# Optimization experiments

Hardware: AMD Instinct MI355X
Metric: run time of the kernel (lower is better)

## Reference

```python
import jax, jax.numpy as jnp
import numpy as np

B, Q, K, DIM, H = 16, 256, 4096, 1024, 16
HD = DIM // H          # head_dim = 64
SCALE = float(np.sqrt(HD))
MAX_QUERIES = 64       # keep_first=True -> kept Q' = MAX_QUERIES + 1


def setup_inputs() -> dict:
    key = jax.random.key(0)
    ks = jax.random.split(key, 8)
    s = 1.0 / np.sqrt(DIM)
    return {
        "q": jax.random.normal(ks[0], (B, Q, DIM), jnp.float32),
        "k": jax.random.normal(ks[1], (B, K, DIM), jnp.float32),
        "v": jax.random.normal(ks[2], (B, K, DIM), jnp.float32),
        "Wq": jax.random.normal(ks[3], (DIM, DIM), jnp.float32) * s,
        "Wk": jax.random.normal(ks[4], (DIM, DIM), jnp.float32) * s,
        "Wv": jax.random.normal(ks[5], (DIM, DIM), jnp.float32) * s,
        "Wo": jax.random.normal(ks[6], (DIM, DIM), jnp.float32) * s,
        "bo": jnp.zeros((DIM,), jnp.float32),
    }


def _split_heads(x):  # [B, L, DIM] -> [B, L, H, HD]
    return x.reshape(x.shape[0], x.shape[1], H, HD)


def reference(q, k, v, Wq, Wk, Wv, Wo, bo):
    # QKV projections (no bias, matching qkv_bias=False; torch Linear is x @ W.T)
    qh = _split_heads(q @ Wq.T)   # [B,Q,H,HD]
    kh = _split_heads(k @ Wk.T)   # [B,K,H,HD]
    vh = _split_heads(v @ Wv.T)   # [B,K,H,HD]

    dots = jnp.einsum("bqhc,bkhc->bhqk", qh / SCALE, kh)  # [B,H,Q,K]

    # select_queries with keep_first=True: stats on detached dots over queries 1:
    sg = jax.lax.stop_gradient(dots)[:, :, 1:, :]          # [B,H,Q-1,K]
    stats = jax.nn.softmax(sg, axis=-2)                    # softmax over query axis
    score = stats.max(axis=(1, 3))                         # amax over (H, K) -> [B, Q-1]
    _, idx = jax.lax.top_k(score, MAX_QUERIES)             # [B, MAX_QUERIES]
    keep = jnp.concatenate(
        [jnp.zeros((dots.shape[0], 1), idx.dtype), idx + 1], axis=-1
    )                                                      # [B, Q'] with Q' = MAX_QUERIES+1

    dots_sel = jnp.take_along_axis(dots, keep[:, None, :, None], axis=2)  # [B,H,Q',K]

    # Competitive softmax: normalize over the (kept) query axis
    attn = jax.nn.softmax(dots_sel, axis=2)                # [B,H,Q',K]

    out = jnp.einsum("bhqk,bkhc->bqhc", attn, vh)          # [B,Q',H,HD]
    out = out.reshape(out.shape[0], out.shape[1], DIM)     # [B,Q',DIM]
    out = out @ Wo.T + bo
    return out, keep
```

## Files before the change

kernel.cpp:

```cpp
#include <hip/hip_runtime.h>
#include <hip/hip_bf16.h>
#include <math.h>

#define B_ 16
#define Q_ 256
#define K_ 4096
#define DIM_ 1024
#define H_ 16
#define HD_ 64
#define MQ_ 64
#define QP_ 65
#define SCALE_INV 0.125f

typedef unsigned short u16;
typedef __attribute__((ext_vector_type(8))) short bf16x8;
typedef __attribute__((ext_vector_type(8))) _Float16 f16x8;
typedef __attribute__((ext_vector_type(8))) short s16x8;
typedef __attribute__((ext_vector_type(4))) float f32x4;

__device__ __forceinline__ u16 f2bf_rne(float f) {
  unsigned u = __float_as_uint(f);
  u += 0x7fffu + ((u >> 16) & 1u);
  return (u16)(u >> 16);
}
__device__ __forceinline__ float bf2f(u16 h) {
  return __uint_as_float(((unsigned)h) << 16);
}
__device__ __forceinline__ u16 f2h_bits(float f) {
  _Float16 h = (_Float16)f;
  return *(u16*)&h;
}
__device__ __forceinline__ f16x8 as_f16x8(s16x8 v) {
  return __builtin_bit_cast(f16x8, v);
}
__device__ __forceinline__ void gload16(const void* g, void* l) {
  __builtin_amdgcn_global_load_lds(
      (const __attribute__((address_space(1))) unsigned int*)g,
      (__attribute__((address_space(3))) unsigned int*)l, 16, 0, 0);
}

__global__ __launch_bounds__(256) void split_bf16(
    const float* __restrict__ x, u16* __restrict__ hi, u16* __restrict__ lo,
    long n8, int wlo) {
  long i = (long)blockIdx.x * 256 + threadIdx.x;
  const long stride = (long)gridDim.x * 256;
  for (; i < n8; i += stride) {
    const float4 a = ((const float4*)x)[2 * i];
    const float4 b = ((const float4*)x)[2 * i + 1];
    const float xs[8] = {a.x, a.y, a.z, a.w, b.x, b.y, b.z, b.w};
    u16 h[8], l[8];
#pragma unroll
    for (int j = 0; j < 8; ++j) {
      h[j] = f2bf_rne(xs[j]);
      l[j] = f2bf_rne(xs[j] - bf2f(h[j]));
    }
    uint4 hv;
    hv.x = h[0] | ((unsigned)h[1] << 16);
    hv.y = h[2] | ((unsigned)h[3] << 16);
    hv.z = h[4] | ((unsigned)h[5] << 16);
    hv.w = h[6] | ((unsigned)h[7] << 16);
    ((uint4*)hi)[i] = hv;
    if (wlo) {
      uint4 lv;
      lv.x = l[0] | ((unsigned)l[1] << 16);
      lv.y = l[2] | ((unsigned)l[3] << 16);
      lv.z = l[4] | ((unsigned)l[5] << 16);
      lv.w = l[6] | ((unsigned)l[7] << 16);
      ((uint4*)lo)[i] = lv;
    }
  }
}

template <int NPROD, int OUTM>
__global__ __launch_bounds__(256) void mfma_gemm_f32a(
    const float* __restrict__ Af,
    const u16* __restrict__ Bhp, const u16* __restrict__ Blp,
    float* __restrict__ C, u16* __restrict__ ChH, u16* __restrict__ ChL) {
  __shared__ u16 Ah_s[128 * 32];
  __shared__ u16 Bh_s[128 * 32];
  __shared__ u16 Al_s[NPROD >= 3 ? 128 * 32 : 16];
  __shared__ u16 Bl_s[NPROD >= 3 ? 128 * 32 : 16];
  const int t = threadIdx.x;
  const int wave = t >> 6;
  const int lane = t & 63;
  const int wr = wave >> 1;
  const int wc = wave & 1;

  int bx = blockIdx.x, by = blockIdx.y;
  if (gridDim.x == 8 && (gridDim.y & 7) == 0) {
    const int flat = by * 8 + bx;
    const int c = flat & 7;
    const int j = flat >> 3;
    by = (j >> 3) * 8 + c;
    bx = j & 7;
  }
  const int n0 = bx * 128;
  const int m0 = by * 128;

  const int sr0 = wave * 32 + (lane >> 2);
  const int sr1 = sr0 + 16;
  const int sw0 = ((sr0 ^ (sr0 >> 2)) & 3) ^ (lane & 3);
  const int sw1 = ((sr1 ^ (sr1 >> 2)) & 3) ^ (lane & 3);
  const size_t gB0 = (size_t)(n0 + sr0) * DIM_ + sw0 * 8;
  const size_t gB1 = (size_t)(n0 + sr1) * DIM_ + sw1 * 8;
  u16* const lB0 = &Bh_s[(wave * 32) * 32];
  u16* const lB1 = &Bh_s[(wave * 32 + 16) * 32];
  u16* const lBl0 = &Bl_s[(wave * 32) * 32];
  u16* const lBl1 = &Bl_s[(wave * 32 + 16) * 32];

  const int ar = t >> 1;
  const int ac0 = (t & 1) * 2;
  const int swzr = (ar ^ (ar >> 2)) & 3;
  const int sl0 = (ac0 ^ swzr) * 8;
  const int sl1 = ((ac0 + 1) ^ swzr) * 8;
  const size_t gA = (size_t)(m0 + ar) * DIM_ + ac0 * 8;

  int aoff[4], boff[4];
#pragma unroll
  for (int m = 0; m < 4; ++m) {
    const int r = wr * 64 + m * 16 + (lane & 15);
    const int p = ((r ^ (r >> 2)) & 3) ^ (lane >> 4);
    aoff[m] = r * 32 + p * 8;
  }
#pragma unroll
  for (int n = 0; n < 4; ++n) {
    const int r = wc * 64 + n * 16 + (lane & 15);
    const int p = ((r ^ (r >> 2)) & 3) ^ (lane >> 4);
    boff[n] = r * 32 + p * 8;
  }

  f32x4 acc[4][4];
#pragma unroll
  for (int m = 0; m < 4; ++m)
#pragma unroll
    for (int n = 0; n < 4; ++n) acc[m][n] = (f32x4)(0.f);

  for (int k0 = 0; k0 < DIM_; k0 += 32) {
    gload16(Bhp + gB0 + k0, lB0);
    gload16(Bhp + gB1 + k0, lB1);
    if (NPROD >= 3) {
      gload16(Blp + gB0 + k0, lBl0);
      gload16(Blp + gB1 + k0, lBl1);
    }
    {
      const float4 a0 = *(const float4*)&Af[gA + k0];
      const float4 a1 = *(const float4*)&Af[gA + k0 + 4];
      const float4 a2 = *(const float4*)&Af[gA + k0 + 8];
      const float4 a3 = *(const float4*)&Af[gA + k0 + 12];
      const float xs[16] = {a0.x, a0.y, a0.z, a0.w, a1.x, a1.y, a1.z, a1.w,
                            a2.x, a2.y, a2.z, a2.w, a3.x, a3.y, a3.z, a3.w};
      u16 h[16], l[16];
#pragma unroll
      for (int j = 0; j < 16; ++j) {
        h[j] = f2bf_rne(xs[j]);
        if (NPROD >= 3) l[j] = f2bf_rne(xs[j] - bf2f(h[j]));
      }
      uint4 hv0, hv1;
      hv0.x = h[0] | ((unsigned)h[1] << 16);  hv0.y = h[2] | ((unsigned)h[3] << 16);
      hv0.z = h[4] | ((unsigned)h[5] << 16);  hv0.w = h[6] | ((unsigned)h[7] << 16);
      hv1.x = h[8] | ((unsigned)h[9] << 16);  hv1.y = h[10] | ((unsigned)h[11] << 16);
      hv1.z = h[12] | ((unsigned)h[13] << 16); hv1.w = h[14] | ((unsigned)h[15] << 16);
      *(uint4*)&Ah_s[ar * 32 + sl0] = hv0;
      *(uint4*)&Ah_s[ar * 32 + sl1] = hv1;
      if (NPROD >= 3) {
        uint4 lv0, lv1;
        lv0.x = l[0] | ((unsigned)l[1] << 16);  lv0.y = l[2] | ((unsigned)l[3] << 16);
        lv0.z = l[4] | ((unsigned)l[5] << 16);  lv0.w = l[6] | ((unsigned)l[7] << 16);
        lv1.x = l[8] | ((unsigned)l[9] << 16);  lv1.y = l[10] | ((unsigned)l[11] << 16);
        lv1.z = l[12] | ((unsigned)l[13] << 16); lv1.w = l[14] | ((unsigned)l[15] << 16);
        *(uint4*)&Al_s[ar * 32 + sl0] = lv0;
        *(uint4*)&Al_s[ar * 32 + sl1] = lv1;
      }
    }
    __syncthreads();
    {
      bf16x8 af[4], bfr[4];
#pragma unroll
      for (int m = 0; m < 4; ++m) af[m] = *(const bf16x8*)&Ah_s[aoff[m]];
#pragma unroll
      for (int n = 0; n < 4; ++n) bfr[n] = *(const bf16x8*)&Bh_s[boff[n]];
#pragma unroll
      for (int m = 0; m < 4; ++m)
#pragma unroll
        for (int n = 0; n < 4; ++n)
          acc[m][n] = __builtin_amdgcn_mfma_f32_16x16x32_bf16(
              af[m], bfr[n], acc[m][n], 0, 0, 0);
      if (NPROD >= 3) {
#pragma unroll
        for (int n = 0; n < 4; ++n) bfr[n] = *(const bf16x8*)&Bl_s[boff[n]];
#pragma unroll
        for (int m = 0; m < 4; ++m)
#pragma unroll
          for (int n = 0; n < 4; ++n)
            acc[m][n] = __builtin_amdgcn_mfma_f32_16x16x32_bf16(
                af[m], bfr[n], acc[m][n], 0, 0, 0);
#pragma unroll
        for (int m = 0; m < 4; ++m) af[m] = *(const bf16x8*)&Al_s[aoff[m]];
#pragma unroll
        for (int n = 0; n < 4; ++n) bfr[n] = *(const bf16x8*)&Bh_s[boff[n]];
#pragma unroll
        for (int m = 0; m < 4; ++m)
#pragma unroll
          for (int n = 0; n < 4; ++n)
            acc[m][n] = __builtin_amdgcn_mfma_f32_16x16x32_bf16(
                af[m], bfr[n], acc[m][n], 0, 0, 0);
      }
    }
    __syncthreads();
  }
#pragma unroll
  for (int m = 0; m < 4; ++m) {
    const int row = m0 + wr * 64 + m * 16 + (lane >> 4) * 4;
#pragma unroll
    for (int n = 0; n < 4; ++n) {
      const int col = n0 + wc * 64 + n * 16 + (lane & 15);
#pragma unroll
      for (int j = 0; j < 4; ++j) {
        const size_t idx = (size_t)(row + j) * DIM_ + col;
        const float a = acc[m][n][j];
        if (OUTM & 1) C[idx] = a;
        if (OUTM & 4) {
          _Float16 hi = (_Float16)a;
          ChH[idx] = *(u16*)&hi;
          if (OUTM & 8) {
            _Float16 lo = (_Float16)(a - (float)hi);
            ChL[idx] = *(u16*)&lo;
          }
        }
      }
    }
  }
}

#define GM 128
#define GN 128
#define GK 16

__global__ __launch_bounds__(256) void gemm_nt(
    const float* __restrict__ A, const float* __restrict__ W,
    float* __restrict__ C, int M, const float* __restrict__ bias,
    u16* __restrict__ hiOut, u16* __restrict__ loOut) {
  __shared__ float As[GK][GM + 4];
  __shared__ float Ws[GK][GN + 4];
  const int t = threadIdx.x;
  const int m0 = blockIdx.x * GM;
  const int n0 = blockIdx.y * GN;
  const int lrow = t >> 2;
  const int lq = (t & 3) * 4;
  const int tm = (t >> 4) * 8;
  const int tn = (t & 15) * 8;
  float acc[8][8];
#pragma unroll
  for (int i = 0; i < 8; ++i)
#pragma unroll
    for (int j = 0; j < 8; ++j) acc[i][j] = 0.f;

  for (int k0 = 0; k0 < DIM_; k0 += GK) {
#pragma unroll
    for (int half = 0; half < 2; ++half) {
      const int row = lrow + half * 64;
      const int gm = m0 + row;
      float4 av = make_float4(0.f, 0.f, 0.f, 0.f);
      if (gm < M) av = *(const float4*)&A[(size_t)gm * DIM_ + k0 + lq];
      As[lq + 0][row] = av.x; As[lq + 1][row] = av.y;
      As[lq + 2][row] = av.z; As[lq + 3][row] = av.w;
      const int gn = n0 + row;
      const float4 wv = *(const float4*)&W[(size_t)gn * DIM_ + k0 + lq];
      Ws[lq + 0][row] = wv.x; Ws[lq + 1][row] = wv.y;
      Ws[lq + 2][row] = wv.z; Ws[lq + 3][row] = wv.w;
    }
    __syncthreads();
#pragma unroll
    for (int kk = 0; kk < GK; ++kk) {
      float a[8], bb[8];
      *(float4*)&a[0] = *(const float4*)&As[kk][tm];
      *(float4*)&a[4] = *(const float4*)&As[kk][tm + 4];
      *(float4*)&bb[0] = *(const float4*)&Ws[kk][tn];
      *(float4*)&bb[4] = *(const float4*)&Ws[kk][tn + 4];
#pragma unroll
      for (int i = 0; i < 8; ++i)
#pragma unroll
        for (int j = 0; j < 8; ++j)
          acc[i][j] = fmaf(a[i], bb[j], acc[i][j]);
    }
    __syncthreads();
  }
#pragma unroll
  for (int i = 0; i < 8; ++i) {
    const int gm = m0 + tm + i;
    if (gm < M) {
      float vals[8];
#pragma unroll
      for (int j = 0; j < 8; ++j) {
        vals[j] = acc[i][j];
        if (bias) vals[j] += bias[n0 + tn + j];
      }
#pragma unroll
      for (int j = 0; j < 8; j += 4) {
        float4 ov;
        ov.x = vals[j + 0]; ov.y = vals[j + 1];
        ov.z = vals[j + 2]; ov.w = vals[j + 3];
        *(float4*)&C[(size_t)gm * DIM_ + n0 + tn + j] = ov;
      }
      if (hiOut) {
        u16 h[8], l[8];
#pragma unroll
        for (int j = 0; j < 8; ++j) {
          _Float16 hh = (_Float16)vals[j];
          _Float16 ll = (_Float16)(vals[j] - (float)hh);
          h[j] = *(u16*)&hh;
          l[j] = *(u16*)&ll;
        }
        uint4 hv, lv;
        hv.x = h[0] | ((unsigned)h[1] << 16); hv.y = h[2] | ((unsigned)h[3] << 16);
        hv.z = h[4] | ((unsigned)h[5] << 16); hv.w = h[6] | ((unsigned)h[7] << 16);
        lv.x = l[0] | ((unsigned)l[1] << 16); lv.y = l[2] | ((unsigned)l[3] << 16);
        lv.z = l[4] | ((unsigned)l[5] << 16); lv.w = l[6] | ((unsigned)l[7] << 16);
        *(uint4*)&hiOut[(size_t)gm * DIM_ + n0 + tn] = hv;
        *(uint4*)&loOut[(size_t)gm * DIM_ + n0 + tn] = lv;
      }
    }
  }
}

__device__ __forceinline__ unsigned fflip(float x) {
  const unsigned u = __float_as_uint(x);
  return (u & 0x80000000u) ? ~u : (u | 0x80000000u);
}

#define AKT 64

__global__ __launch_bounds__(256) void pass_a_mfma(
    const u16* __restrict__ qhH, const u16* __restrict__ qhL,
    const u16* __restrict__ khH, const u16* __restrict__ khL,
    unsigned* __restrict__ sbuf) {
  __shared__ u16 KsH[AKT * 72];
  __shared__ u16 KsL[AKT * 72];
  __shared__ float red[4][2 * AKT];
  const int bx = blockIdx.x;
  const int b = bx >> 7;
  const int h = (bx >> 3) & 15;
  const int ks0 = (bx & 7) * (K_ / 8);
  const int t = threadIdx.x;
  const int w = t >> 6;
  const int l = t & 63;
  const int g = l >> 4;
  const int a15 = l & 15;

  f16x8 qA[2][4][2];
#pragma unroll
  for (int mt = 0; mt < 4; ++mt) {
    const int qrow = w * 64 + mt * 16 + a15;
    const size_t base = ((size_t)(b * Q_ + qrow)) * DIM_ + h * HD_;
#pragma unroll
    for (int ks = 0; ks < 2; ++ks) {
      qA[0][mt][ks] = *(const f16x8*)&qhH[base + ks * 32 + g * 8];
      qA[1][mt][ks] = *(const f16x8*)&qhL[base + ks * 32 + g * 8];
    }
  }
  float rmax[4][4];
#pragma unroll
  for (int mt = 0; mt < 4; ++mt)
#pragma unroll
    for (int j = 0; j < 4; ++j) rmax[mt][j] = -3.4e38f;

  for (int k0 = ks0; k0 < ks0 + K_ / 8; k0 += AKT) {
    uint4 sH[2], sL[2];
    int sr[2], sc[2];
#pragma unroll
    for (int s = 0; s < 2; ++s) {
      const int c = t + 256 * s;
      sr[s] = c >> 3;
      sc[s] = c & 7;
      const size_t gidx =
          ((size_t)(b * K_ + k0 + sr[s])) * DIM_ + h * HD_ + sc[s] * 8;
      sH[s] = *(const uint4*)&khH[gidx];
      sL[s] = *(const uint4*)&khL[gidx];
    }
    __syncthreads();
#pragma unroll
    for (int s = 0; s < 2; ++s) {
      *(uint4*)&KsH[sr[s] * 72 + sc[s] * 8] = sH[s];
      *(uint4*)&KsL[sr[s] * 72 + sc[s] * 8] = sL[s];
    }
    __syncthreads();

    f32x4 acc[4][4];
#pragma unroll
    for (int mt = 0; mt < 4; ++mt)
#pragma unroll
      for (int kt = 0; kt < 4; ++kt) acc[mt][kt] = (f32x4)(0.f);
#pragma unroll
    for (int ks = 0; ks < 2; ++ks) {
#pragma unroll
      for (int kt = 0; kt < 4; ++kt) {
        const f16x8 bH =
            *(const f16x8*)&KsH[(kt * 16 + a15) * 72 + ks * 32 + g * 8];
        const f16x8 bL =
            *(const f16x8*)&KsL[(kt * 16 + a15) * 72 + ks * 32 + g * 8];
#pragma unroll
        for (int mt = 0; mt < 4; ++mt) {
          acc[mt][kt] = __builtin_amdgcn_mfma_f32_16x16x32_f16(
              qA[0][mt][ks], bH, acc[mt][kt], 0, 0, 0);
          acc[mt][kt] = __builtin_amdgcn_mfma_f32_16x16x32_f16(
              qA[0][mt][ks], bL, acc[mt][kt], 0, 0, 0);
          acc[mt][kt] = __builtin_amdgcn_mfma_f32_16x16x32_f16(
              qA[1][mt][ks], bH, acc[mt][kt], 0, 0, 0);
        }
      }
    }
#pragma unroll
    for (int mt = 0; mt < 4; ++mt)
#pragma unroll
      for (int kt = 0; kt < 4; ++kt) acc[mt][kt] = acc[mt][kt] * 0.125f;

    float cmax[4];
#pragma unroll
    for (int kt = 0; kt < 4; ++kt) {
      float m = -3.4e38f;
#pragma unroll
      for (int mt = 0; mt < 4; ++mt)
#pragma unroll
        for (int j = 0; j < 4; ++j) {
          const bool ex = (w == 0) & (mt == 0) & (g == 0) & (j == 0);
          if (!ex) m = fmaxf(m, acc[mt][kt][j]);
        }
      m = fmaxf(m, __shfl_xor(m, 16, 64));
      m = fmaxf(m, __shfl_xor(m, 32, 64));
      cmax[kt] = m;
    }
    if (l < 16) {
#pragma unroll
      for (int kt = 0; kt < 4; ++kt) red[w][kt * 16 + l] = cmax[kt];
    }
    __syncthreads();
#pragma unroll
    for (int kt = 0; kt < 4; ++kt)
      cmax[kt] = fmaxf(fmaxf(red[0][kt * 16 + a15], red[1][kt * 16 + a15]),
                       fmaxf(red[2][kt * 16 + a15], red[3][kt * 16 + a15]));
    float csum[4];
#pragma unroll
    for (int kt = 0; kt < 4; ++kt) {
      float s = 0.f;
#pragma unroll
      for (int mt = 0; mt < 4; ++mt)
#pragma unroll
        for (int j = 0; j < 4; ++j) {
          const bool ex = (w == 0) & (mt == 0) & (g == 0) & (j == 0);
          if (!ex) s += __expf(acc[mt][kt][j] - cmax[kt]);
        }
      s += __shfl_xor(s, 16, 64);
      s += __shfl_xor(s, 32, 64);
      csum[kt] = s;
    }
    if (l < 16) {
#pragma unroll
      for (int kt = 0; kt < 4; ++kt) red[w][AKT + kt * 16 + l] = csum[kt];
    }
    __syncthreads();
    float lse[4];
#pragma unroll
    for (int kt = 0; kt < 4; ++kt) {
      const float s = red[0][AKT + kt * 16 + a15] + red[1][AKT + kt * 16 + a15] +
                      red[2][AKT + kt * 16 + a15] + red[3][AKT + kt * 16 + a15];
      lse[kt] = cmax[kt] + logf(s);
    }
#pragma unroll
    for (int mt = 0; mt < 4; ++mt)
#pragma unroll
      for (int j = 0; j < 4; ++j) {
        float v = -3.4e38f;
#pragma unroll
        for (int kt = 0; kt < 4; ++kt)
          v = fmaxf(v, acc[mt][kt][j] - lse[kt]);
        v = fmaxf(v, __shfl_xor(v, 1, 64));
        v = fmaxf(v, __shfl_xor(v, 2, 64));
        v = fmaxf(v, __shfl_xor(v, 4, 64));
        v = fmaxf(v, __shfl_xor(v, 8, 64));
        rmax[mt][j] = fmaxf(rmax[mt][j], v);
      }
  }
  if (a15 == 0) {
#pragma unroll
    for (int mt = 0; mt < 4; ++mt)
#pragma unroll
      for (int j = 0; j < 4; ++j) {
        const int qi = w * 64 + mt * 16 + g * 4 + j;
        if (qi > 0) atomicMax(&sbuf[b * Q_ + qi], fflip(rmax[mt][j]));
      }
  }
}

#define KT 64
#define DC 32
#define KSPLIT 8

__global__ __launch_bounds__(256) void pass_a(
    const float* __restrict__ qh, const float* __restrict__ kh,
    unsigned* __restrict__ sbuf) {
  __shared__ float qs[DC][Q_ + 4];
  __shared__ float ksm[DC][KT + 4];
  __shared__ float red[32][KT + 1];
  __shared__ float cmax[KT];
  __shared__ float clse[KT];
  const int blk = blockIdx.x;
  const int b = blk >> 7;
  const int h = (blk >> 3) & 15;
  const int ks0 = (blk & 7) * (K_ / KSPLIT);
  const int t = threadIdx.x;
  const int tq = t >> 3;
  const int tk = t & 7;
  float rmax[8];
#pragma unroll
  for (int i = 0; i < 8; ++i) rmax[i] = -3.4e38f;

  for (int k0 = ks0; k0 < ks0 + K_ / KSPLIT; k0 += KT) {
    float acc[8][8];
#pragma unroll
    for (int i = 0; i < 8; ++i)
#pragma unroll
      for (int j = 0; j < 8; ++j) acc[i][j] = 0.f;

    for (int dc = 0; dc < HD_; dc += DC) {
      {
        const float* src = &qh[((size_t)(b * Q_ + t)) * DIM_ + h * HD_ + dc];
#pragma unroll
        for (int u = 0; u < DC / 4; ++u) {
          const float4 vv = *(const float4*)&src[u * 4];
          qs[u * 4 + 0][t] = vv.x * SCALE_INV;
          qs[u * 4 + 1][t] = vv.y * SCALE_INV;
          qs[u * 4 + 2][t] = vv.z * SCALE_INV;
          qs[u * 4 + 3][t] = vv.w * SCALE_INV;
        }
      }
      {
        const int r = t >> 2;
        const int qd = (t & 3) * 8;
        const float* src =
            &kh[((size_t)(b * K_ + k0 + r)) * DIM_ + h * HD_ + dc + qd];
#pragma unroll
        for (int u = 0; u < 2; ++u) {
          const float4 vv = *(const float4*)&src[u * 4];
          ksm[qd + u * 4 + 0][r] = vv.x; ksm[qd + u * 4 + 1][r] = vv.y;
          ksm[qd + u * 4 + 2][r] = vv.z; ksm[qd + u * 4 + 3][r] = vv.w;
        }
      }
      __syncthreads();
#pragma unroll
      for (int d = 0; d < DC; ++d) {
        float a[8], bb[8];
        *(float4*)&a[0] = *(const float4*)&qs[d][tq * 8];
        *(float4*)&a[4] = *(const float4*)&qs[d][tq * 8 + 4];
        *(float4*)&bb[0] = *(const float4*)&ksm[d][tk * 8];
        *(float4*)&bb[4] = *(const float4*)&ksm[d][tk * 8 + 4];
#pragma unroll
        for (int i = 0; i < 8; ++i)
#pragma unroll
          for (int j = 0; j < 8; ++j)
            acc[i][j] = fmaf(a[i], bb[j], acc[i][j]);
      }
      __syncthreads();
    }
#pragma unroll
    for (int j = 0; j < 8; ++j) {
      float m = -3.4e38f;
#pragma unroll
      for (int i = 0; i < 8; ++i) {
        if (tq == 0 && i == 0) continue;
        m = fmaxf(m, acc[i][j]);
      }
      red[tq][tk * 8 + j] = m;
    }
    __syncthreads();
    if (t < KT) {
      float m = -3.4e38f;
      for (int g = 0; g < 32; ++g) m = fmaxf(m, red[g][t]);
      cmax[t] = m;
    }
    __syncthreads();
#pragma unroll
    for (int j = 0; j < 8; ++j) {
      const float m = cmax[tk * 8 + j];
      float s = 0.f;
#pragma unroll
      for (int i = 0; i < 8; ++i) {
        if (tq == 0 && i == 0) continue;
        s += __expf(acc[i][j] - m);
      }
      red[tq][tk * 8 + j] = s;
    }
    __syncthreads();
    if (t < KT) {
      float s = 0.f;
      for (int g = 0; g < 32; ++g) s += red[g][t];
      clse[t] = cmax[t] + logf(s);
    }
    __syncthreads();
#pragma unroll
    for (int i = 0; i < 8; ++i) {
      float v = -3.4e38f;
#pragma unroll
      for (int j = 0; j < 8; ++j) v = fmaxf(v, acc[i][j] - clse[tk * 8 + j]);
      v = fmaxf(v, __shfl_xor(v, 1, 64));
      v = fmaxf(v, __shfl_xor(v, 2, 64));
      v = fmaxf(v, __shfl_xor(v, 4, 64));
      rmax[i] = fmaxf(rmax[i], v);
    }
    __syncthreads();
  }
  if (tk == 0) {
#pragma unroll
    for (int i = 0; i < 8; ++i) {
      const int qi = tq * 8 + i;
      if (qi > 0) atomicMax(&sbuf[b * Q_ + qi], fflip(rmax[i]));
    }
  }
}

__global__ void topk_kernel(const unsigned* __restrict__ sbuf,
                            int* __restrict__ keep, float* __restrict__ keepf) {
  const int b = blockIdx.x;
  const int lane = threadIdx.x;
  unsigned long long pk[4];
#pragma unroll
  for (int j = 0; j < 4; ++j) {
    const int q = 1 + lane + 64 * j;
    if (q <= 255) {
      const unsigned s = sbuf[b * Q_ + q];
      pk[j] = (((unsigned long long)s) << 32) | (unsigned)(256 - q);
    } else {
      pk[j] = 0ull;
    }
  }
  if (lane == 0) { keep[b * QP_] = 0; keepf[b * QP_] = 0.f; }
  for (int it = 0; it < MQ_; ++it) {
    unsigned long long best = pk[0];
#pragma unroll
    for (int j = 1; j < 4; ++j) best = (pk[j] > best) ? pk[j] : best;
    for (int m = 1; m < 64; m <<= 1) {
      const unsigned long long o = __shfl_xor(best, m, 64);
      best = (o > best) ? o : best;
    }
    const int q = 256 - (int)(best & 0xffffffffu);
#pragma unroll
    for (int j = 0; j < 4; ++j)
      if (pk[j] == best) pk[j] = 0ull;
    if (lane == 0) {
      keep[b * QP_ + 1 + it] = q;
      keepf[b * QP_ + 1 + it] = (float)q;
    }
  }
}

#define PSPL 4

__global__ __launch_bounds__(256) void pass_b_mfma(
    const float* __restrict__ qh, const u16* __restrict__ khb,
    const u16* __restrict__ vhb, const int* __restrict__ keep,
    float* __restrict__ part) {
  __shared__ __align__(16) char SH[72960];
  u16* const Qs = (u16*)SH;
  u16* const Ks = (u16*)(SH + 11520);
  u16* const Vs = (u16*)(SH + 29952);
  u16* const Ps = (u16*)(SH + 47360);
  float* const osum = (float*)(SH + 11520);

  const int bx = blockIdx.x;
  const int b = bx >> 6;
  const int h = (bx >> 2) & 15;
  const int sp = bx & 3;
  const int t = threadIdx.x;
  const int w = t >> 6;
  const int l = t & 63;
  const int g = l >> 4;
  const int a15 = l & 15;

  for (int idx = t; idx < 80 * 8; idx += 256) {
    const int row = idx >> 3, ch = idx & 7;
    uint4 pk;
    if (row < QP_) {
      const int kq = keep[b * QP_ + row];
      const float* src = &qh[((size_t)(b * Q_ + kq)) * DIM_ + h * HD_ + ch * 8];
      const float4 x0 = *(const float4*)&src[0];
      const float4 x1 = *(const float4*)&src[4];
      pk.x = f2h_bits(x0.x * SCALE_INV) | ((unsigned)f2h_bits(x0.y * SCALE_INV) << 16);
      pk.y = f2h_bits(x0.z * SCALE_INV) | ((unsigned)f2h_bits(x0.w * SCALE_INV) << 16);
      pk.z = f2h_bits(x1.x * SCALE_INV) | ((unsigned)f2h_bits(x1.y * SCALE_INV) << 16);
      pk.w = f2h_bits(x1.z * SCALE_INV) | ((unsigned)f2h_bits(x1.w * SCALE_INV) << 16);
    } else {
      pk = make_uint4(0, 0, 0, 0);
    }
    *(uint4*)&Qs[row * 72 + ch * 8] = pk;
  }
  __syncthreads();

  f32x4 oacc[5][4];
#pragma unroll
  for (int mt = 0; mt < 5; ++mt)
#pragma unroll
    for (int dt = 0; dt < 4; ++dt) oacc[mt][dt] = (f32x4)(0.f);

  const int kt0 = sp * (K_ / PSPL);
  for (int kt = 0; kt < K_ / PSPL; kt += 128) {
    const int k0 = kt0 + kt;
    uint4 kreg[4], vreg[4];
    int srow[4], sch[4];
#pragma unroll
    for (int s = 0; s < 4; ++s) {
      const int c = t + 256 * s;
      srow[s] = c >> 3;
      sch[s] = c & 7;
      const size_t gidx =
          ((size_t)(b * K_ + k0 + srow[s])) * DIM_ + h * HD_ + sch[s] * 8;
      kreg[s] = *(const uint4*)&khb[gidx];
      vreg[s] = *(const uint4*)&vhb[gidx];
    }
    __syncthreads();
#pragma unroll
    for (int s = 0; s < 4; ++s) {
      *(uint4*)&Ks[srow[s] * 72 + sch[s] * 8] = kreg[s];
      uint2 v0; v0.x = vreg[s].x; v0.y = vreg[s].y;
      uint2 v1; v1.x = vreg[s].z; v1.y = vreg[s].w;
      *(uint2*)&Vs[srow[s] * 68 + sch[s] * 8] = v0;
      *(uint2*)&Vs[srow[s] * 68 + sch[s] * 8 + 4] = v1;
    }
    __syncthreads();

    f32x4 S[5][2];
#pragma unroll
    for (int mt = 0; mt < 5; ++mt)
#pragma unroll
      for (int nt = 0; nt < 2; ++nt) S[mt][nt] = (f32x4)(0.f);
#pragma unroll
    for (int kk = 0; kk < 2; ++kk) {
      f16x8 aq[5];
#pragma unroll
      for (int mt = 0; mt < 5; ++mt)
        aq[mt] = *(const f16x8*)&Qs[(mt * 16 + a15) * 72 + kk * 32 + g * 8];
#pragma unroll
      for (int nt = 0; nt < 2; ++nt) {
        const f16x8 bk =
            *(const f16x8*)&Ks[(w * 32 + nt * 16 + a15) * 72 + kk * 32 + g * 8];
#pragma unroll
        for (int mt = 0; mt < 5; ++mt)
          S[mt][nt] = __builtin_amdgcn_mfma_f32_16x16x32_f16(aq[mt], bk,
                                                             S[mt][nt], 0, 0, 0);
      }
    }
#pragma unroll
    for (int nt = 0; nt < 2; ++nt) {
      float m = -3.4e38f;
#pragma unroll
      for (int mt = 0; mt < 5; ++mt)
#pragma unroll
        for (int j = 0; j < 4; ++j) {
          const bool valid = (mt < 4) | ((g == 0) & (j == 0));
          if (valid) m = fmaxf(m, S[mt][nt][j]);
        }
      m = fmaxf(m, __shfl_xor(m, 16, 64));
      m = fmaxf(m, __shfl_xor(m, 32, 64));
      float s = 0.f;
#pragma unroll
      for (int mt = 0; mt < 5; ++mt)
#pragma unroll
        for (int j = 0; j < 4; ++j) {
          const bool valid = (mt < 4) | ((g == 0) & (j == 0));
          const float p = valid ? __expf(S[mt][nt][j] - m) : 0.f;
          S[mt][nt][j] = p;
          s += p;
        }
      s += __shfl_xor(s, 16, 64);
      s += __shfl_xor(s, 32, 64);
      const float r = 1.f / s;
#pragma unroll
      for (int mt = 0; mt < 5; ++mt)
#pragma unroll
        for (int j = 0; j < 4; ++j)
          Ps[w * 3200 + (mt * 16 + g * 4 + j) * 40 + nt * 16 + a15] =
              f2h_bits(S[mt][nt][j] * r);
    }
    f16x8 ap[5];
#pragma unroll
    for (int mt = 0; mt < 5; ++mt)
      ap[mt] = *(const f16x8*)&Ps[w * 3200 + (mt * 16 + a15) * 40 + g * 8];
#pragma unroll
    for (int dt = 0; dt < 4; ++dt) {
      s16x8 bv;
#pragma unroll
      for (int e = 0; e < 8; ++e)
        bv[e] = (short)Vs[(w * 32 + g * 8 + e) * 68 + dt * 16 + a15];
#pragma unroll
      for (int mt = 0; mt < 5; ++mt)
        oacc[mt][dt] = __builtin_amdgcn_mfma_f32_16x16x32_f16(
            ap[mt], as_f16x8(bv), oacc[mt][dt], 0, 0, 0);
    }
  }

#pragma unroll
  for (int dt = 0; dt < 4; ++dt) {
    __syncthreads();
#pragma unroll
    for (int mt = 0; mt < 5; ++mt)
#pragma unroll
      for (int j = 0; j < 4; ++j)
        osum[w * 1360 + (mt * 16 + g * 4 + j) * 17 + a15] = oacc[mt][dt][j];
    __syncthreads();
    for (int idx = t; idx < QP_ * 16; idx += 256) {
      const int q = idx >> 4, c = idx & 15;
      const float sm = osum[q * 17 + c] + osum[1360 + q * 17 + c] +
                       osum[2720 + q * 17 + c] + osum[4080 + q * 17 + c];
      part[(((size_t)sp * B_ + b) * QP_ + q) * DIM_ + h * 64 + dt * 16 + c] = sm;
    }
  }
}

__global__ __launch_bounds__(256) void pass_b(
    const float* __restrict__ qh, const float* __restrict__ kh,
    const float* __restrict__ vh, const int* __restrict__ keep,
    float* __restrict__ part) {
  __shared__ float qs[QP_][HD_ + 4];
  __shared__ float kv[KT][HD_ + 4];
  __shared__ float att[QP_][KT + 4];
  __shared__ float cmax[KT];
  __shared__ float crcp[KT];
  const int bx = blockIdx.x;
  const int b = bx >> 6;
  const int h = (bx >> 2) & 15;
  const int sp = bx & 3;
  const int t = threadIdx.x;

  if (t < QP_) {
    const int kq = keep[b * QP_ + t];
    const float* src = &qh[((size_t)(b * Q_ + kq)) * DIM_ + h * HD_];
#pragma unroll
    for (int u = 0; u < HD_ / 4; ++u) {
      float4 vv = *(const float4*)&src[u * 4];
      vv.x *= SCALE_INV; vv.y *= SCALE_INV;
      vv.z *= SCALE_INV; vv.w *= SCALE_INV;
      *(float4*)&qs[t][u * 4] = vv;
    }
  }
  const int c = t & 63;
  const int jg = t >> 6;
  const int j0 = jg * 17;
  const int j1 = (jg == 3) ? QP_ : (j0 + 17);
  const int j2 = t >> 2;
  const int cg = (t & 3) * 16;
  const int r = t >> 2;
  const int qd = (t & 3) * 16;
  float oacc[16], oacc2[16];
#pragma unroll
  for (int u = 0; u < 16; ++u) { oacc[u] = 0.f; oacc2[u] = 0.f; }

  __syncthreads();

  const int kbeg = sp * (K_ / PSPL);
  const int kend = kbeg + K_ / PSPL;
  for (int k0 = kbeg; k0 < kend; k0 += KT) {
    {
      const float* src = &kh[((size_t)(b * K_ + k0 + r)) * DIM_ + h * HD_ + qd];
#pragma unroll
      for (int u = 0; u < 4; ++u)
        *(float4*)&kv[r][qd + u * 4] = *(const float4*)&src[u * 4];
    }
    __syncthreads();
    {
      float4 kr[16];
#pragma unroll
      for (int u = 0; u < 16; ++u) kr[u] = *(const float4*)&kv[c][u * 4];
      for (int j = j0; j < j1; ++j) {
        float4 s4 = make_float4(0.f, 0.f, 0.f, 0.f);
#pragma unroll
        for (int u = 0; u < 16; ++u) {
          const float4 qv = *(const float4*)&qs[j][u * 4];
          s4.x = fmaf(qv.x, kr[u].x, s4.x);
          s4.y = fmaf(qv.y, kr[u].y, s4.y);
          s4.z = fmaf(qv.z, kr[u].z, s4.z);
          s4.w = fmaf(qv.w, kr[u].w, s4.w);
        }
        att[j][c] = (s4.x + s4.y) + (s4.z + s4.w);
      }
    }
    __syncthreads();
    {
      const float* src = &vh[((size_t)(b * K_ + k0 + r)) * DIM_ + h * HD_ + qd];
#pragma unroll
      for (int u = 0; u < 4; ++u)
        *(float4*)&kv[r][qd + u * 4] = *(const float4*)&src[u * 4];
      if (t < KT) {
        float m = att[0][t];
        for (int j = 1; j < QP_; ++j) m = fmaxf(m, att[j][t]);
        float s = 0.f;
        for (int j = 0; j < QP_; ++j) s += __expf(att[j][t] - m);
        cmax[t] = m;
        crcp[t] = 1.f / s;
      }
    }
    __syncthreads();
    for (int e = t; e < QP_ * KT; e += 256) {
      const int jj = e >> 6;
      const int cc = e & 63;
      att[jj][cc] = __expf(att[jj][cc] - cmax[cc]) * crcp[cc];
    }
    __syncthreads();
    {
      for (int ck = 0; ck < KT; ++ck) {
        const float a = att[j2][ck];
#pragma unroll
        for (int u = 0; u < 4; ++u) {
          const float4 vv = *(const float4*)&kv[ck][cg + u * 4];
          oacc[u * 4 + 0] = fmaf(a, vv.x, oacc[u * 4 + 0]);
          oacc[u * 4 + 1] = fmaf(a, vv.y, oacc[u * 4 + 1]);
          oacc[u * 4 + 2] = fmaf(a, vv.z, oacc[u * 4 + 2]);
          oacc[u * 4 + 3] = fmaf(a, vv.w, oacc[u * 4 + 3]);
        }
      }
      if (t < 4) {
        const int cg2 = t * 16;
        for (int ck = 0; ck < KT; ++ck) {
          const float a = att[64][ck];
#pragma unroll
          for (int u = 0; u < 4; ++u) {
            const float4 vv = *(const float4*)&kv[ck][cg2 + u * 4];
            oacc2[u * 4 + 0] = fmaf(a, vv.x, oacc2[u * 4 + 0]);
            oacc2[u * 4 + 1] = fmaf(a, vv.y, oacc2[u * 4 + 1]);
            oacc2[u * 4 + 2] = fmaf(a, vv.z, oacc2[u * 4 + 2]);
            oacc2[u * 4 + 3] = fmaf(a, vv.w, oacc2[u * 4 + 3]);
          }
        }
      }
    }
    __syncthreads();
  }
  {
    float* dst =
        &part[(((size_t)sp * B_ + b) * QP_ + j2) * DIM_ + h * HD_ + cg];
    *(float4*)&dst[0] = make_float4(oacc[0], oacc[1], oacc[2], oacc[3]);
    *(float4*)&dst[4] = make_float4(oacc[4], oacc[5], oacc[6], oacc[7]);
    *(float4*)&dst[8] = make_float4(oacc[8], oacc[9], oacc[10], oacc[11]);
    *(float4*)&dst[12] = make_float4(oacc[12], oacc[13], oacc[14], oacc[15]);
    if (t < 4) {
      float* dst2 =
          &part[(((size_t)sp * B_ + b) * QP_ + 64) * DIM_ + h * HD_ + t * 16];
      *(float4*)&dst2[0] = make_float4(oacc2[0], oacc2[1], oacc2[2], oacc2[3]);
      *(float4*)&dst2[4] = make_float4(oacc2[4], oacc2[5], oacc2[6], oacc2[7]);
      *(float4*)&dst2[8] = make_float4(oacc2[8], oacc2[9], oacc2[10], oacc2[11]);
      *(float4*)&dst2[12] = make_float4(oacc2[12], oacc2[13], oacc2[14], oacc2[15]);
    }
  }
}

__global__ __launch_bounds__(256) void reduce_part(
    const float* __restrict__ part, float* __restrict__ opre) {
  const long n4 = (long)B_ * QP_ * DIM_ / 4;
  const long i = (long)blockIdx.x * 256 + threadIdx.x;
  if (i >= n4) return;
  float4 s = ((const float4*)part)[i];
#pragma unroll
  for (int sp = 1; sp < PSPL; ++sp) {
    const float4 p = ((const float4*)part)[(long)sp * n4 + i];
    s.x += p.x; s.y += p.y; s.z += p.z; s.w += p.w;
  }
  ((float4*)opre)[i] = s;
}

extern "C" void kernel_launch(void* const* d_in, const int* in_sizes, int n_in,
                              void* d_out, int out_size, void* d_ws, size_t ws_size,
                              hipStream_t stream) {
  const float* q  = (const float*)d_in[0];
  const float* k  = (const float*)d_in[1];
  const float* v  = (const float*)d_in[2];
  const float* Wq = (const float*)d_in[3];
  const float* Wk = (const float*)d_in[4];
  const float* Wv = (const float*)d_in[5];
  const float* Wo = (const float*)d_in[6];
  const float* bo = (const float*)d_in[7];
  float* out = (float*)d_out;

  char* base = (char*)d_ws;
  size_t off = 0;
  auto alloc = [&](size_t bytes) {
    char* p = base + off;
    off = (off + bytes + 255) & ~(size_t)255;
    return (void*)p;
  };
  float* qh   = (float*)alloc((size_t)B_ * Q_ * DIM_ * 4);
  float* opre = (float*)alloc((size_t)B_ * QP_ * DIM_ * 4);
  unsigned* sbuf = (unsigned*)alloc((size_t)B_ * Q_ * 4);
  int* keep   = (int*)alloc((size_t)B_ * QP_ * 4);
  const size_t common_off = off;
  u16* qhH = (u16*)alloc((size_t)B_ * Q_ * DIM_ * 2);
  u16* qhL = (u16*)alloc((size_t)B_ * Q_ * DIM_ * 2);
  u16* khH = (u16*)alloc((size_t)B_ * K_ * DIM_ * 2);
  u16* khL = (u16*)alloc((size_t)B_ * K_ * DIM_ * 2);
  u16* vhH = (u16*)alloc((size_t)B_ * K_ * DIM_ * 2);
  u16* wHi = (u16*)alloc((size_t)DIM_ * DIM_ * 2);
  u16* wLo = (u16*)alloc((size_t)DIM_ * DIM_ * 2);
  float* partBig = (float*)alloc((size_t)PSPL * B_ * QP_ * DIM_ * 4);
  const bool big = (off <= ws_size);
  float* keepf = out + (size_t)B_ * QP_ * DIM_;
  const dim3 blk(256);

  hipMemsetAsync(sbuf, 0, B_ * Q_ * sizeof(unsigned), stream);

  if (big) {
    const long nW8 = (long)DIM_ * DIM_ / 8;
    split_bf16<<<512, blk, 0, stream>>>(Wk, wHi, wLo, nW8, 1);
    mfma_gemm_f32a<3, 12><<<dim3(DIM_ / 128, B_ * K_ / 128), blk, 0, stream>>>(
        k, wHi, wLo, nullptr, khH, khL);
    split_bf16<<<512, blk, 0, stream>>>(Wv, wHi, nullptr, nW8, 0);
    mfma_gemm_f32a<1, 4><<<dim3(DIM_ / 128, B_ * K_ / 128), blk, 0, stream>>>(
        v, wHi, nullptr, nullptr, vhH, nullptr);
    gemm_nt<<<dim3(B_ * Q_ / GM, DIM_ / GN), blk, 0, stream>>>(
        q, Wq, qh, B_ * Q_, nullptr, qhH, qhL);
    pass_a_mfma<<<dim3(B_ * H_ * 8), blk, 0, stream>>>(qhH, qhL, khH, khL, sbuf);
    topk_kernel<<<dim3(B_), dim3(64), 0, stream>>>(sbuf, keep, keepf);
    pass_b_mfma<<<dim3(B_ * H_ * PSPL), blk, 0, stream>>>(qh, khH, vhH, keep, partBig);
    reduce_part<<<dim3((B_ * QP_ * DIM_ / 4 + 255) / 256), blk, 0, stream>>>(partBig, opre);
    gemm_nt<<<dim3((B_ * QP_ + GM - 1) / GM, DIM_ / GN), blk, 0, stream>>>(
        opre, Wo, out, B_ * QP_, bo, nullptr, nullptr);
  } else {
    off = common_off;
    float* kh = (float*)alloc((size_t)B_ * K_ * DIM_ * 4);
    float* vh = (float*)alloc((size_t)B_ * K_ * DIM_ * 4);
    float* part = (float*)alloc((size_t)PSPL * B_ * QP_ * DIM_ * 4);
    gemm_nt<<<dim3(B_ * K_ / GM, DIM_ / GN), blk, 0, stream>>>(
        k, Wk, kh, B_ * K_, nullptr, nullptr, nullptr);
    gemm_nt<<<dim3(B_ * K_ / GM, DIM_ / GN), blk, 0, stream>>>(
        v, Wv, vh, B_ * K_, nullptr, nullptr, nullptr);
    gemm_nt<<<dim3(B_ * Q_ / GM, DIM_ / GN), blk, 0, stream>>>(
        q, Wq, qh, B_ * Q_, nullptr, nullptr, nullptr);
    pass_a<<<dim3(B_ * H_ * KSPLIT), blk, 0, stream>>>(qh, kh, sbuf);
    topk_kernel<<<dim3(B_), dim3(64), 0, stream>>>(sbuf, keep, keepf);
    pass_b<<<dim3(B_ * H_ * PSPL), blk, 0, stream>>>(qh, kh, vh, keep, part);
    reduce_part<<<dim3((B_ * QP_ * DIM_ / 4 + 255) / 256), blk, 0, stream>>>(part, opre);
    gemm_nt<<<dim3((B_ * QP_ + GM - 1) / GM, DIM_ / GN), blk, 0, stream>>>(
        opre, Wo, out, B_ * QP_, bo, nullptr, nullptr);
  }
}
```

Baseline: 1.510 ms.

## Fuse K and V projections into one MFMA GEMM with pre-split K input

Replaces the two separate K and V projection GEMMs with one kernel that computes both accumulators per tile. The K input is pre-split into bf16 hi/lo planes by a separate pass and loaded via direct-to-LDS loads, while V is still converted in-kernel. The aim is to share launch and scheduling overhead and reduce per-tile conversion work. In exchange it adds a full pass over K that writes two extra large bf16 arrays, doubles accumulator registers (possible occupancy loss), and reuses the K split buffer as the partials buffer.

Result: slower. 2.088 ms (+38.2%).

```diff
diff --git a/kernel.cpp b/kernel.cpp
--- a/kernel.cpp
+++ b/kernel.cpp
@@ -71,15 +71,18 @@
   }
 }
 
-template <int NPROD, int OUTM>
-__global__ __launch_bounds__(256) void mfma_gemm_f32a(
-    const float* __restrict__ Af,
+__global__ __launch_bounds__(256) void mfma_gemm_kv(
+    const u16* __restrict__ Ahp, const u16* __restrict__ Alp,
+    const float* __restrict__ Vf,
     const u16* __restrict__ Bhp, const u16* __restrict__ Blp,
-    float* __restrict__ C, u16* __restrict__ ChH, u16* __restrict__ ChL) {
+    const u16* __restrict__ Bvp,
+    u16* __restrict__ KhH, u16* __restrict__ KhL, u16* __restrict__ VhH) {
   __shared__ u16 Ah_s[128 * 32];
+  __shared__ u16 Al_s[128 * 32];
   __shared__ u16 Bh_s[128 * 32];
-  __shared__ u16 Al_s[NPROD >= 3 ? 128 * 32 : 16];
-  __shared__ u16 Bl_s[NPROD >= 3 ? 128 * 32 : 16];
+  __shared__ u16 Bl_s[128 * 32];
+  __shared__ u16 Av_s[128 * 32];
+  __shared__ u16 Bv_s[128 * 32];
   const int t = threadIdx.x;
   const int wave = t >> 6;
   const int lane = t & 63;
@@ -101,19 +104,27 @@
   const int sr1 = sr0 + 16;
   const int sw0 = ((sr0 ^ (sr0 >> 2)) & 3) ^ (lane & 3);
   const int sw1 = ((sr1 ^ (sr1 >> 2)) & 3) ^ (lane & 3);
+  const size_t gA0 = (size_t)(m0 + sr0) * DIM_ + sw0 * 8;
+  const size_t gA1 = (size_t)(m0 + sr1) * DIM_ + sw1 * 8;
   const size_t gB0 = (size_t)(n0 + sr0) * DIM_ + sw0 * 8;
   const size_t gB1 = (size_t)(n0 + sr1) * DIM_ + sw1 * 8;
+  u16* const lA0 = &Ah_s[(wave * 32) * 32];
+  u16* const lA1 = &Ah_s[(wave * 32 + 16) * 32];
+  u16* const lAl0 = &Al_s[(wave * 32) * 32];
+  u16* const lAl1 = &Al_s[(wave * 32 + 16) * 32];
   u16* const lB0 = &Bh_s[(wave * 32) * 32];
   u16* const lB1 = &Bh_s[(wave * 32 + 16) * 32];
   u16* const lBl0 = &Bl_s[(wave * 32) * 32];
   u16* const lBl1 = &Bl_s[(wave * 32 + 16) * 32];
+  u16* const lBv0 = &Bv_s[(wave * 32) * 32];
+  u16* const lBv1 = &Bv_s[(wave * 32 + 16) * 32];
 
   const int ar = t >> 1;
   const int ac0 = (t & 1) * 2;
   const int swzr = (ar ^ (ar >> 2)) & 3;
   const int sl0 = (ac0 ^ swzr) * 8;
   const int sl1 = ((ac0 + 1) ^ swzr) * 8;
-  const size_t gA = (size_t)(m0 + ar) * DIM_ + ac0 * 8;
+  const size_t gV = (size_t)(m0 + ar) * DIM_ + ac0 * 8;
 
   int aoff[4], boff[4];
 #pragma unroll
@@ -129,48 +140,43 @@
     boff[n] = r * 32 + p * 8;
   }
 
-  f32x4 acc[4][4];
+  f32x4 accK[4][4], accV[4][4];
 #pragma unroll
   for (int m = 0; m < 4; ++m)
 #pragma unroll
-    for (int n = 0; n < 4; ++n) acc[m][n] = (f32x4)(0.f);
+    for (int n = 0; n < 4; ++n) {
+      accK[m][n] = (f32x4)(0.f);
+      accV[m][n] = (f32x4)(0.f);
+    }
 
   for (int k0 = 0; k0 < DIM_; k0 += 32) {
+    gload16(Ahp + gA0 + k0, lA0);
+    gload16(Ahp + gA1 + k0, lA1);
+    gload16(Alp + gA0 + k0, lAl0);
+    gload16(Alp + gA1 + k0, lAl1);
     gload16(Bhp + gB0 + k0, lB0);
     gload16(Bhp + gB1 + k0, lB1);
-    if (NPROD >= 3) {
-      gload16(Blp + gB0 + k0, lBl0);
-      gload16(Blp + gB1 + k0, lBl1);
-    }
+    gload16(Blp + gB0 + k0, lBl0);
+    gload16(Blp + gB1 + k0, lBl1);
+    gload16(Bvp + gB0 + k0, lBv0);
+    gload16(Bvp + gB1 + k0, lBv1);
     {
-      const float4 a0 = *(const float4*)&Af[gA + k0];
-      const float4 a1 = *(const float4*)&Af[gA + k0 + 4];
-      const float4 a2 = *(const float4*)&Af[gA + k0 + 8];
-      const float4 a3 = *(const float4*)&Af[gA + k0 + 12];
+      const float4 a0 = *(const float4*)&Vf[gV + k0];
+      const float4 a1 = *(const float4*)&Vf[gV + k0 + 4];
+      const float4 a2 = *(const float4*)&Vf[gV + k0 + 8];
+      const float4 a3 = *(const float4*)&Vf[gV + k0 + 12];
       const float xs[16] = {a0.x, a0.y, a0.z, a0.w, a1.x, a1.y, a1.z, a1.w,
                             a2.x, a2.y, a2.z, a2.w, a3.x, a3.y, a3.z, a3.w};
-      u16 h[16], l[16];
-#pragma unroll
-      for (int j = 0; j < 16; ++j) {
-        h[j] = f2bf_rne(xs[j]);
-        if (NPROD >= 3) l[j] = f2bf_rne(xs[j] - bf2f(h[j]));
-      }
+      u16 h[16];
+#pragma unroll
+      for (int j = 0; j < 16; ++j) h[j] = f2bf_rne(xs[j]);
       uint4 hv0, hv1;
       hv0.x = h[0] | ((unsigned)h[1] << 16);  hv0.y = h[2] | ((unsigned)h[3] << 16);
       hv0.z = h[4] | ((unsigned)h[5] << 16);  hv0.w = h[6] | ((unsigned)h[7] << 16);
       hv1.x = h[8] | ((unsigned)h[9] << 16);  hv1.y = h[10] | ((unsigned)h[11] << 16);
       hv1.z = h[12] | ((unsigned)h[13] << 16); hv1.w = h[14] | ((unsigned)h[15] << 16);
-      *(uint4*)&Ah_s[ar * 32 + sl0] = hv0;
-      *(uint4*)&Ah_s[ar * 32 + sl1] = hv1;
-      if (NPROD >= 3) {
-        uint4 lv0, lv1;
-        lv0.x = l[0] | ((unsigned)l[1] << 16);  lv0.y = l[2] | ((unsigned)l[3] << 16);
-        lv0.z = l[4] | ((unsigned)l[5] << 16);  lv0.w = l[6] | ((unsigned)l[7] << 16);
-        lv1.x = l[8] | ((unsigned)l[9] << 16);  lv1.y = l[10] | ((unsigned)l[11] << 16);
-        lv1.z = l[12] | ((unsigned)l[13] << 16); lv1.w = l[14] | ((unsigned)l[15] << 16);
-        *(uint4*)&Al_s[ar * 32 + sl0] = lv0;
-        *(uint4*)&Al_s[ar * 32 + sl1] = lv1;
-      }
+      *(uint4*)&Av_s[ar * 32 + sl0] = hv0;
+      *(uint4*)&Av_s[ar * 32 + sl1] = hv1;
     }
     __syncthreads();
     {
@@ -183,28 +189,36 @@
       for (int m = 0; m < 4; ++m)
 #pragma unroll
         for (int n = 0; n < 4; ++n)
-          acc[m][n] = __builtin_amdgcn_mfma_f32_16x16x32_bf16(
-              af[m], bfr[n], acc[m][n], 0, 0, 0);
-      if (NPROD >= 3) {
-#pragma unroll
-        for (int n = 0; n < 4; ++n) bfr[n] = *(const bf16x8*)&Bl_s[boff[n]];
-#pragma unroll
-        for (int m = 0; m < 4; ++m)
-#pragma unroll
-          for (int n = 0; n < 4; ++n)
-            acc[m][n] = __builtin_amdgcn_mfma_f32_16x16x32_bf16(
-                af[m], bfr[n], acc[m][n], 0, 0, 0);
-#pragma unroll
-        for (int m = 0; m < 4; ++m) af[m] = *(const bf16x8*)&Al_s[aoff[m]];
-#pragma unroll
-        for (int n = 0; n < 4; ++n) bfr[n] = *(const bf16x8*)&Bh_s[boff[n]];
-#pragma unroll
-        for (int m = 0; m < 4; ++m)
-#pragma unroll
-          for (int n = 0; n < 4; ++n)
-            acc[m][n] = __builtin_amdgcn_mfma_f32_16x16x32_bf16(
-                af[m], bfr[n], acc[m][n], 0, 0, 0);
-      }
+          accK[m][n] = __builtin_amdgcn_mfma_f32_16x16x32_bf16(
+              af[m], bfr[n], accK[m][n], 0, 0, 0);
+#pragma unroll
+      for (int n = 0; n < 4; ++n) bfr[n] = *(const bf16x8*)&Bl_s[boff[n]];
+#pragma unroll
+      for (int m = 0; m < 4; ++m)
+#pragma unroll
+        for (int n = 0; n < 4; ++n)
+          accK[m][n] = __builtin_amdgcn_mfma_f32_16x16x32_bf16(
+              af[m], bfr[n], accK[m][n], 0, 0, 0);
+#pragma unroll
+      for (int m = 0; m < 4; ++m) af[m] = *(const bf16x8*)&Al_s[aoff[m]];
+#pragma unroll
+      for (int n = 0; n < 4; ++n) bfr[n] = *(const bf16x8*)&Bh_s[boff[n]];
+#pragma unroll
+      for (int m = 0; m < 4; ++m)
+#pragma unroll
+        for (int n = 0; n < 4; ++n)
+          accK[m][n] = __builtin_amdgcn_mfma_f32_16x16x32_bf16(
+              af[m], bfr[n], accK[m][n], 0, 0, 0);
+#pragma unroll
+      for (int m = 0; m < 4; ++m) af[m] = *(const bf16x8*)&Av_s[aoff[m]];
+#pragma unroll
+      for (int n = 0; n < 4; ++n) bfr[n] = *(const bf16x8*)&Bv_s[boff[n]];
+#pragma unroll
+      for (int m = 0; m < 4; ++m)
+#pragma unroll
+        for (int n = 0; n < 4; ++n)
+          accV[m][n] = __builtin_amdgcn_mfma_f32_16x16x32_bf16(
+              af[m], bfr[n], accV[m][n], 0, 0, 0);
     }
     __syncthreads();
   }
@@ -217,16 +231,12 @@
 #pragma unroll
       for (int j = 0; j < 4; ++j) {
         const size_t idx = (size_t)(row + j) * DIM_ + col;
-        const float a = acc[m][n][j];
-        if (OUTM & 1) C[idx] = a;
-        if (OUTM & 4) {
-          _Float16 hi = (_Float16)a;
-          ChH[idx] = *(u16*)&hi;
-          if (OUTM & 8) {
-            _Float16 lo = (_Float16)(a - (float)hi);
-            ChL[idx] = *(u16*)&lo;
-          }
-        }
+        const float aK = accK[m][n][j];
+        _Float16 hi = (_Float16)aK;
+        KhH[idx] = *(u16*)&hi;
+        _Float16 lo = (_Float16)(aK - (float)hi);
+        KhL[idx] = *(u16*)&lo;
+        VhH[idx] = f2h_bits(accV[m][n][j]);
       }
     }
   }
@@ -994,9 +1004,11 @@
   u16* khH = (u16*)alloc((size_t)B_ * K_ * DIM_ * 2);
   u16* khL = (u16*)alloc((size_t)B_ * K_ * DIM_ * 2);
   u16* vhH = (u16*)alloc((size_t)B_ * K_ * DIM_ * 2);
-  u16* wHi = (u16*)alloc((size_t)DIM_ * DIM_ * 2);
-  u16* wLo = (u16*)alloc((size_t)DIM_ * DIM_ * 2);
-  float* partBig = (float*)alloc((size_t)PSPL * B_ * QP_ * DIM_ * 4);
+  u16* kHi = (u16*)alloc((size_t)B_ * K_ * DIM_ * 2);
+  u16* kLo = (u16*)alloc((size_t)B_ * K_ * DIM_ * 2);
+  u16* wkHi = (u16*)alloc((size_t)DIM_ * DIM_ * 2);
+  u16* wkLo = (u16*)alloc((size_t)DIM_ * DIM_ * 2);
+  u16* wvHi = (u16*)alloc((size_t)DIM_ * DIM_ * 2);
   const bool big = (off <= ws_size);
   float* keepf = out + (size_t)B_ * QP_ * DIM_;
   const dim3 blk(256);
@@ -1004,19 +1016,20 @@
   hipMemsetAsync(sbuf, 0, B_ * Q_ * sizeof(unsigned), stream);
 
   if (big) {
+    float* part = (float*)kHi;
+    const long nKV8 = (long)B_ * K_ * DIM_ / 8;
     const long nW8 = (long)DIM_ * DIM_ / 8;
-    split_bf16<<<512, blk, 0, stream>>>(Wk, wHi, wLo, nW8, 1);
-    mfma_gemm_f32a<3, 12><<<dim3(DIM_ / 128, B_ * K_ / 128), blk, 0, stream>>>(
-        k, wHi, wLo, nullptr, khH, khL);
-    split_bf16<<<512, blk, 0, stream>>>(Wv, wHi, nullptr, nW8, 0);
-    mfma_gemm_f32a<1, 4><<<dim3(DIM_ / 128, B_ * K_ / 128), blk, 0, stream>>>(
-        v, wHi, nullptr, nullptr, vhH, nullptr);
+    split_bf16<<<2048, blk, 0, stream>>>(k, kHi, kLo, nKV8, 1);
+    split_bf16<<<512, blk, 0, stream>>>(Wk, wkHi, wkLo, nW8, 1);
+    split_bf16<<<512, blk, 0, stream>>>(Wv, wvHi, nullptr, nW8, 0);
+    mfma_gemm_kv<<<dim3(DIM_ / 128, B_ * K_ / 128), blk, 0, stream>>>(
+        kHi, kLo, v, wkHi, wkLo, wvHi, khH, khL, vhH);
     gemm_nt<<<dim3(B_ * Q_ / GM, DIM_ / GN), blk, 0, stream>>>(
         q, Wq, qh, B_ * Q_, nullptr, qhH, qhL);
     pass_a_mfma<<<dim3(B_ * H_ * 8), blk, 0, stream>>>(qhH, qhL, khH, khL, sbuf);
     topk_kernel<<<dim3(B_), dim3(64), 0, stream>>>(sbuf, keep, keepf);
-    pass_b_mfma<<<dim3(B_ * H_ * PSPL), blk, 0, stream>>>(qh, khH, vhH, keep, partBig);
-    reduce_part<<<dim3((B_ * QP_ * DIM_ / 4 + 255) / 256), blk, 0, stream>>>(partBig, opre);
+    pass_b_mfma<<<dim3(B_ * H_ * PSPL), blk, 0, stream>>>(qh, khH, vhH, keep, part);
+    reduce_part<<<dim3((B_ * QP_ * DIM_ / 4 + 255) / 256), blk, 0, stream>>>(part, opre);
     gemm_nt<<<dim3((B_ * QP_ + GM - 1) / GM, DIM_ / GN), blk, 0, stream>>>(
         opre, Wo, out, B_ * QP_, bo, nullptr, nullptr);
   } else {
```
